# Performance work log

Hardware: AMD Instinct MI355X
Metric: run time of the kernel (lower is better)

Reference implementation:

```python
import jax, jax.numpy as jnp
import numpy as np

# Static conv hyperparameters (match init_kwargs)
STRIDE = (1, 1)
PAD = (1, 1)
DIL = (1, 1)
GROUPS = 1
DG = 1  # num_deformable_groups


def setup_inputs() -> dict:
    key = jax.random.key(0)
    k1, k2, k3 = jax.random.split(key, 3)
    B, C, H, W = 4, 256, 64, 64
    OC, kh, kw = 256, 3, 3
    x = jax.random.normal(k1, (B, C, H, W), dtype=jnp.float32)
    # offset: [B, DG*2*kh*kw, Ho, Wo], ordered (tap, [dy, dx]) per deformable group
    offset = jax.random.normal(k2, (B, DG * 2 * kh * kw, H, W), dtype=jnp.float32)
    n = C * kh * kw
    stdv = 1.0 / np.sqrt(n)
    weight = jax.random.uniform(k3, (OC, C // GROUPS, kh, kw), dtype=jnp.float32,
                                minval=-stdv, maxval=stdv)
    return {"x": x, "offset": offset, "weight": weight}


def _deform_conv(x, offset, weight):
    B, C, H, W = x.shape
    OC, Cg_w, kh, kw = weight.shape
    sh, sw = STRIDE
    ph, pw = PAD
    dh, dw = DIL
    Ho = (H + 2 * ph - (dh * (kh - 1) + 1)) // sh + 1
    Wo = (W + 2 * pw - (dw * (kw - 1) + 1)) // sw + 1
    K = kh * kw
    Cg = C // DG  # channels per deformable group

    # offsets: [B, DG, K, 2, Ho, Wo]; channel 0 = dy (h), channel 1 = dx (w)
    off = offset.reshape(B, DG, K, 2, Ho, Wo)

    # base (undeformed) sampling positions per tap
    ki, kj = jnp.meshgrid(jnp.arange(kh), jnp.arange(kw), indexing='ij')
    base_h = (jnp.arange(Ho) * sh - ph)[None, :] + (ki.reshape(-1) * dh)[:, None]  # [K, Ho]
    base_w = (jnp.arange(Wo) * sw - pw)[None, :] + (kj.reshape(-1) * dw)[:, None]  # [K, Wo]

    pos_h = base_h[None, None, :, :, None].astype(x.dtype) + off[:, :, :, 0]  # [B,DG,K,Ho,Wo]
    pos_w = base_w[None, None, :, None, :].astype(x.dtype) + off[:, :, :, 1]  # [B,DG,K,Ho,Wo]

    h0f = jnp.floor(pos_h)
    w0f = jnp.floor(pos_w)
    lh = pos_h - h0f  # fractional parts
    lw = pos_w - w0f
    h0 = h0f.astype(jnp.int32)
    w0 = w0f.astype(jnp.int32)

    xg = x.reshape(B, DG, Cg, H * W)

    def gather(hi, wi):
        # zero-padded gather: out-of-range corners contribute 0 (mmcv DCNv1 semantics)
        valid = (hi >= 0) & (hi < H) & (wi >= 0) & (wi < W)  # [B,DG,K,Ho,Wo]
        idx = jnp.clip(hi, 0, H - 1) * W + jnp.clip(wi, 0, W - 1)
        flat = idx.reshape(B, DG, 1, K * Ho * Wo)
        vals = jnp.take_along_axis(
            xg, jnp.broadcast_to(flat, (B, DG, Cg, K * Ho * Wo)), axis=3)
        vals = vals.reshape(B, DG, Cg, K, Ho, Wo)
        return vals * valid[:, :, None].astype(x.dtype)

    # bilinear interpolation over 4 corners -> im2col columns [B,DG,Cg,K,Ho,Wo]
    cols = (gather(h0, w0) * ((1 - lh) * (1 - lw))[:, :, None]
            + gather(h0, w0 + 1) * ((1 - lh) * lw)[:, :, None]
            + gather(h0 + 1, w0) * (lh * (1 - lw))[:, :, None]
            + gather(h0 + 1, w0 + 1) * (lh * lw)[:, :, None])

    # grouped GEMM: columns x weight
    cols = cols.reshape(B, GROUPS, C // GROUPS, K, Ho, Wo)
    wg = weight.reshape(GROUPS, OC // GROUPS, Cg_w, K)
    out = jnp.einsum('gock,bgckhw->bgohw', wg, cols)
    return out.reshape(B, OC, Ho, Wo)


def reference(x, offset, weight):
    return _deform_conv(x, offset, weight)
```

## Files before the change

kernel.cpp:

```cpp
#include <hip/hip_runtime.h>
#include <hip/hip_bf16.h>
#include <math.h>


constexpr int B  = 4;
constexpr int C  = 256;
constexpr int H  = 64;
constexpr int W  = 64;
constexpr int OC = 256;
constexpr int Ho = 64;
constexpr int Wo = 64;

constexpr int NT     = 64;
constexpr int CHUNKS = 72;
constexpr int WROW   = 40;

constexpr size_t WA_ELTS  = (size_t)CHUNKS * OC * WROW;
constexpr size_t XB_ELTS  = (size_t)B * 8 * 4096 * 32;
constexpr size_t OUT_ELTS = (size_t)B * OC * Ho * Wo;

typedef __attribute__((ext_vector_type(8))) short bf16x8;
typedef __attribute__((ext_vector_type(4))) float f32x4;

__device__ __forceinline__ float bf_lo(unsigned u) {
    union { unsigned i; float f; } c; c.i = u << 16; return c.f;
}
__device__ __forceinline__ float bf_hi(unsigned u) {
    union { unsigned i; float f; } c; c.i = u & 0xffff0000u; return c.f;
}
__device__ __forceinline__ ushort fbf(float f) {
    __hip_bfloat16 h = __float2bfloat16(f); return *(ushort*)&h;
}

__global__ __launch_bounds__(256)
void prep_all(const float* __restrict__ x, const float* __restrict__ wt,
              ushort* __restrict__ xb, ushort* __restrict__ wA)
{
    __shared__ ushort sx[128 * WROW];
    __shared__ ushort sw[CHUNKS * WROW];
    const int t = threadIdx.x;

    if (blockIdx.x < 1024) {
        const int blk = blockIdx.x;
        const int hwb = blk & 31;
        const int cb  = (blk >> 5) & 7;
        const int b   = blk >> 8;
        const int hw0 = hwb << 7;
        const int lhw = t & 127, chalf = t >> 7;
        #pragma unroll
        for (int i = 0; i < 16; ++i) {
            const int c = i * 2 + chalf;
            sx[lhw * WROW + c] =
                fbf(x[(((size_t)(b * 256 + cb * 32 + c)) << 12) + hw0 + lhw]);
        }
        __syncthreads();
        const int whw = t >> 1, wh = t & 1;
        const uint4 v0 = *(const uint4*)&sx[whw * WROW + wh * 16];
        const uint4 v1 = *(const uint4*)&sx[whw * WROW + wh * 16 + 8];
        uint4* dst = (uint4*)(xb + ((size_t)((b * 8 + cb) * 4096 + hw0) << 5));
        dst[whw * 4 + wh * 2 + 0] = v0;
        dst[whw * 4 + wh * 2 + 1] = v1;
    } else {
        const int oc = blockIdx.x - 1024;
        const int c  = t, chb = c >> 5, kk = c & 31;
        const float* wp = wt + ((size_t)oc * C + c) * 9;
        #pragma unroll
        for (int tap = 0; tap < 9; ++tap)
            sw[(tap * 8 + chb) * WROW + kk] = fbf(wp[tap]);
        if (c < CHUNKS) {
            #pragma unroll
            for (int j = 0; j < 8; ++j) sw[c * WROW + 32 + j] = 0;
        }
        __syncthreads();
        const uint4* sv = (const uint4*)sw;
        for (int i = c; i < CHUNKS * 5; i += 256) {
            const int row = i / 5, q = i % 5;
            ((uint4*)(wA + ((size_t)row * OC + oc) * WROW))[q] = sv[i];
        }
    }
}

__global__ __launch_bounds__(512, 1)
void dcn_mfma(const ushort* __restrict__ xb, const float* __restrict__ off,
              const ushort* __restrict__ wA_g, float* __restrict__ po)
{
    __shared__ __align__(16) ushort s_wA[OC * WROW];
    __shared__ __align__(16) ushort s_col[NT * WROW];
    __shared__ int2   s_midx[9 * NT];
    __shared__ float4 s_mw[9 * NT];

    const int xcd = blockIdx.x & 7;
    const int ii  = blockIdx.x >> 3;
    const int b   = xcd & 3;
    const int khalf = ii & 1;
    const int ho  = ((xcd >> 2) << 5) + (ii >> 1);
    const int ch0 = khalf * 36, ch1 = ch0 + 36;
    float* outp = po + (size_t)khalf * OUT_ELTS;
    const int tid = threadIdx.x;

    for (int s = tid; s < 9 * NT; s += 512) {
        const int n   = s & 63;
        const int tap = s >> 6;
        const float dy = off[((size_t)(b * 18 + 2 * tap)     * Ho + ho) * Wo + n];
        const float dx = off[((size_t)(b * 18 + 2 * tap + 1) * Ho + ho) * Wo + n];
        const float ph = (float)(ho - 1 + tap / 3) + dy;
        const float pw = (float)(n  - 1 + tap % 3) + dx;
        const float h0f = floorf(ph), w0f = floorf(pw);
        const int h0 = (int)h0f, w0 = (int)w0f;
        const float lh = ph - h0f, lw = pw - w0f;
        const int wb = min(max(w0, 0), W - 2);
        const int ht = min(max(h0, 0), H - 1);
        const int hb = min(max(h0 + 1, 0), H - 1);
        const float s0 = (wb == w0) ? (1.f - lw) : ((wb == w0 + 1) ? lw : 0.f);
        const float s1 = (wb + 1 == w0 + 1) ? lw : ((wb + 1 == w0) ? (1.f - lw) : 0.f);
        const float wtp = (h0 >= 0 && h0 < H)         ? (1.f - lh) : 0.f;
        const float wbt = (h0 + 1 >= 0 && h0 + 1 < H) ? lh         : 0.f;
        s_midx[s] = make_int2(ht * W + wb, hb * W + wb);
        s_mw[s]   = make_float4(wtp * s0, wtp * s1, wbt * s0, wbt * s1);
    }

    const int lane = tid & 63;
    const int wv   = tid >> 6;
    const int ocb  = wv >> 1;
    const int phh  = wv & 1;
    const int kq   = lane >> 4;
    const int mr   = lane & 15;

    const int sm_tid = tid - 256;
    const int sn  = sm_tid >> 2;
    const int sgg = sm_tid & 3;

    f32x4 acc[4][2];
    #pragma unroll
    for (int mt = 0; mt < 4; ++mt)
        #pragma unroll
        for (int nt = 0; nt < 2; ++nt)
            acc[mt][nt] = (f32x4){0.f, 0.f, 0.f, 0.f};

    for (int ch = ch0; ch < ch1; ++ch) {
        __syncthreads();

        if (tid < 256) {
            #pragma unroll
            for (int i = 0; i < 5; ++i) {
                const int seg = wv * 5 + i;
                __builtin_amdgcn_global_load_lds(
                    (const __attribute__((address_space(1))) void*)
                        (wA_g + (size_t)ch * OC * WROW + seg * 512 + lane * 8),
                    (__attribute__((address_space(3))) void*)&s_wA[seg * 512],
                    16, 0, 0);
            }
        } else {
            const int tap = ch >> 3;
            const int cb  = ch & 7;
            const int2   mi = s_midx[tap * NT + sn];
            const float4 mw = s_mw[tap * NT + sn];
            const ushort* xp = xb + ((size_t)(b * 8 + cb) << 17) + (sgg << 3);
            const uint4 c00 = *(const uint4*)(xp + ((size_t)mi.x << 5));
            const uint4 c01 = *(const uint4*)(xp + (((size_t)mi.x + 1) << 5));
            const uint4 c10 = *(const uint4*)(xp + ((size_t)mi.y << 5));
            const uint4 c11 = *(const uint4*)(xp + (((size_t)mi.y + 1) << 5));
            union { ushort pk[8]; uint4 v; } u;
            const unsigned a00[4] = {c00.x, c00.y, c00.z, c00.w};
            const unsigned a01[4] = {c01.x, c01.y, c01.z, c01.w};
            const unsigned a10[4] = {c10.x, c10.y, c10.z, c10.w};
            const unsigned a11[4] = {c11.x, c11.y, c11.z, c11.w};
            #pragma unroll
            for (int j = 0; j < 4; ++j) {
                const float vlo = mw.x * bf_lo(a00[j]) + mw.y * bf_lo(a01[j])
                                + mw.z * bf_lo(a10[j]) + mw.w * bf_lo(a11[j]);
                const float vhi = mw.x * bf_hi(a00[j]) + mw.y * bf_hi(a01[j])
                                + mw.z * bf_hi(a10[j]) + mw.w * bf_hi(a11[j]);
                u.pk[2 * j]     = fbf(vlo);
                u.pk[2 * j + 1] = fbf(vhi);
            }
            *(uint4*)&s_col[sn * WROW + sgg * 8] = u.v;
        }
        __syncthreads();

        bf16x8 bfr[2];
        #pragma unroll
        for (int nt = 0; nt < 2; ++nt)
            bfr[nt] = *(const bf16x8*)&s_col[((phh * 2 + nt) * 16 + mr) * WROW + kq * 8];
        #pragma unroll
        for (int mt = 0; mt < 4; ++mt) {
            const bf16x8 afr = *(const bf16x8*)&s_wA[(ocb * 64 + mt * 16 + mr) * WROW + kq * 8];
            #pragma unroll
            for (int nt = 0; nt < 2; ++nt)
                acc[mt][nt] = __builtin_amdgcn_mfma_f32_16x16x32_bf16(afr, bfr[nt], acc[mt][nt], 0, 0, 0);
        }
    }

    #pragma unroll
    for (int mt = 0; mt < 4; ++mt)
        #pragma unroll
        for (int nt = 0; nt < 2; ++nt)
            #pragma unroll
            for (int r = 0; r < 4; ++r) {
                const int oc = ocb * 64 + mt * 16 + kq * 4 + r;
                const int wo = (phh * 2 + nt) * 16 + mr;
                outp[((size_t)(b * OC + oc) * Ho + ho) * Wo + wo] = acc[mt][nt][r];
            }
}

__global__ __launch_bounds__(256)
void reduce2(const float4* __restrict__ p0, const float4* __restrict__ p1,
             float4* __restrict__ out)
{
    const int i = blockIdx.x * 256 + threadIdx.x;
    const float4 a = p0[i], b = p1[i];
    out[i] = make_float4(a.x + b.x, a.y + b.y, a.z + b.z, a.w + b.w);
}

extern "C" void kernel_launch(void* const* d_in, const int* in_sizes, int n_in,
                              void* d_out, int out_size, void* d_ws, size_t ws_size,
                              hipStream_t stream)
{
    const float* x   = (const float*)d_in[0];
    const float* off = (const float*)d_in[1];
    const float* wt  = (const float*)d_in[2];
    float* out = (float*)d_out;

    ushort* wA = (ushort*)d_ws;
    ushort* xb = wA + WA_ELTS;
    float*  po = (float*)(xb + XB_ELTS);

    prep_all<<<1280, 256, 0, stream>>>(x, wt, xb, wA);
    dcn_mfma<<<512, 512, 0, stream>>>(xb, off, wA, po);
    reduce2<<<(int)(OUT_ELTS / 4 / 256), 256, 0, stream>>>(
        (const float4*)po, (const float4*)(po + OUT_ELTS), (float4*)out);
}
```

Before: 120.9 us.

## Double-buffer weight DMA and gather staging with register prefetch pipeline

Splits the per-chunk loop into a two-stage software pipeline. Weights are DMA'd into alternating LDS buffers one chunk ahead, and sampler threads issue the next chunk's global gathers into registers before interpolating the current one. Fixed waitcnt counts, raw s_barrier and sched_barrier replace __syncthreads so loads overlap the MFMA phase. Launch bounds are raised to allow more blocks per CU despite doubled LDS use, which adds register pressure and relies on hand-tuned vmcnt values being correct.

Result: no change. 121.6 us (+0.6%).

```diff
diff --git a/kernel.cpp b/kernel.cpp
--- a/kernel.cpp
+++ b/kernel.cpp
@@ -80,21 +80,23 @@
     }
 }
 
-__global__ __launch_bounds__(512, 1)
+struct GathRegs { uint4 c00, c01, c10, c11; float4 mw; };
+
+__global__ __launch_bounds__(512, 4)
 void dcn_mfma(const ushort* __restrict__ xb, const float* __restrict__ off,
               const ushort* __restrict__ wA_g, float* __restrict__ po)
 {
-    __shared__ __align__(16) ushort s_wA[OC * WROW];
-    __shared__ __align__(16) ushort s_col[NT * WROW];
-    __shared__ int2   s_midx[9 * NT];
-    __shared__ float4 s_mw[9 * NT];
+    __shared__ __align__(16) ushort s_wA[2][OC * WROW];
+    __shared__ __align__(16) ushort s_col[2][NT * WROW];
+    __shared__ __align__(16) float4 s_mw[9 * NT];
+    __shared__ __align__(8)  int2   s_midx[9 * NT];
 
     const int xcd = blockIdx.x & 7;
     const int ii  = blockIdx.x >> 3;
     const int b   = xcd & 3;
     const int khalf = ii & 1;
     const int ho  = ((xcd >> 2) << 5) + (ii >> 1);
-    const int ch0 = khalf * 36, ch1 = ch0 + 36;
+    const int ch0 = khalf * 36;
     float* outp = po + (size_t)khalf * OUT_ELTS;
     const int tid = threadIdx.x;
 
@@ -125,10 +127,12 @@
     const int phh  = wv & 1;
     const int kq   = lane >> 4;
     const int mr   = lane & 15;
+    const bool is_w = (tid < 256);
 
     const int sm_tid = tid - 256;
     const int sn  = sm_tid >> 2;
     const int sgg = sm_tid & 3;
+    const ushort* xb_sg = xb + ((size_t)b << 20) + (sgg << 3);
 
     f32x4 acc[4][2];
     #pragma unroll
@@ -137,58 +141,97 @@
         for (int nt = 0; nt < 2; ++nt)
             acc[mt][nt] = (f32x4){0.f, 0.f, 0.f, 0.f};
 
-    for (int ch = ch0; ch < ch1; ++ch) {
-        __syncthreads();
-
-        if (tid < 256) {
-            #pragma unroll
-            for (int i = 0; i < 5; ++i) {
-                const int seg = wv * 5 + i;
-                __builtin_amdgcn_global_load_lds(
-                    (const __attribute__((address_space(1))) void*)
-                        (wA_g + (size_t)ch * OC * WROW + seg * 512 + lane * 8),
-                    (__attribute__((address_space(3))) void*)&s_wA[seg * 512],
-                    16, 0, 0);
+    auto dmaw = [&](int ch, int buf) {
+        #pragma unroll
+        for (int i = 0; i < 5; ++i) {
+            const int seg = wv * 5 + i;
+            __builtin_amdgcn_global_load_lds(
+                (const __attribute__((address_space(1))) void*)
+                    (wA_g + (size_t)ch * OC * WROW + seg * 512 + lane * 8),
+                (__attribute__((address_space(3))) void*)&s_wA[buf][seg * 512],
+                16, 0, 0);
+        }
+    };
+    auto issueg = [&](int ch, GathRegs& g) {
+        const int tap = ch >> 3;
+        const int cb  = ch & 7;
+        const int2 mi = s_midx[tap * NT + sn];
+        g.mw = s_mw[tap * NT + sn];
+        const ushort* xp = xb_sg + ((size_t)cb << 17);
+        g.c00 = *(const uint4*)(xp + ((size_t)mi.x << 5));
+        g.c01 = *(const uint4*)(xp + (((size_t)mi.x + 1) << 5));
+        g.c10 = *(const uint4*)(xp + ((size_t)mi.y << 5));
+        g.c11 = *(const uint4*)(xp + (((size_t)mi.y + 1) << 5));
+    };
+    auto sampfma = [&](const GathRegs& g, int buf) {
+        union { ushort pk[8]; uint4 v; } u;
+        const unsigned a00[4] = {g.c00.x, g.c00.y, g.c00.z, g.c00.w};
+        const unsigned a01[4] = {g.c01.x, g.c01.y, g.c01.z, g.c01.w};
+        const unsigned a10[4] = {g.c10.x, g.c10.y, g.c10.z, g.c10.w};
+        const unsigned a11[4] = {g.c11.x, g.c11.y, g.c11.z, g.c11.w};
+        #pragma unroll
+        for (int j = 0; j < 4; ++j) {
+            const float vlo = g.mw.x * bf_lo(a00[j]) + g.mw.y * bf_lo(a01[j])
+                            + g.mw.z * bf_lo(a10[j]) + g.mw.w * bf_lo(a11[j]);
+            const float vhi = g.mw.x * bf_hi(a00[j]) + g.mw.y * bf_hi(a01[j])
+                            + g.mw.z * bf_hi(a10[j]) + g.mw.w * bf_hi(a11[j]);
+            u.pk[2 * j]     = fbf(vlo);
+            u.pk[2 * j + 1] = fbf(vhi);
+        }
+        *(uint4*)&s_col[buf][sn * WROW + sgg * 8] = u.v;
+    };
+    auto mfmaph = [&](int buf) {
+        const bf16x8 bfr0 = *(const bf16x8*)&s_col[buf][((phh * 2 + 0) * 16 + mr) * WROW + kq * 8];
+        const bf16x8 bfr1 = *(const bf16x8*)&s_col[buf][((phh * 2 + 1) * 16 + mr) * WROW + kq * 8];
+        #pragma unroll
+        for (int mt = 0; mt < 4; ++mt) {
+            const bf16x8 afr = *(const bf16x8*)&s_wA[buf][(ocb * 64 + mt * 16 + mr) * WROW + kq * 8];
+            acc[mt][0] = __builtin_amdgcn_mfma_f32_16x16x32_bf16(afr, bfr0, acc[mt][0], 0, 0, 0);
+            acc[mt][1] = __builtin_amdgcn_mfma_f32_16x16x32_bf16(afr, bfr1, acc[mt][1], 0, 0, 0);
+        }
+    };
+
+    __syncthreads();
+
+    GathRegs gA, gB;
+    if (is_w) dmaw(ch0, 0);
+    else      issueg(ch0, gA);
+
+    #pragma unroll 1
+    for (int it = 0; it < 18; ++it) {
+        const int ch = ch0 + 2 * it;
+
+        if (is_w) {
+            dmaw(ch + 1, 1);
+            asm volatile("s_waitcnt vmcnt(5)" ::: "memory");
+        } else {
+            issueg(ch + 1, gB);
+            sampfma(gA, 0);
+            asm volatile("s_waitcnt lgkmcnt(0)" ::: "memory");
+        }
+        __builtin_amdgcn_s_barrier();
+        __builtin_amdgcn_sched_barrier(0);
+        mfmaph(0);
+        __builtin_amdgcn_sched_barrier(0);
+        __builtin_amdgcn_s_barrier();
+
+        if (is_w) {
+            if (it < 17) {
+                dmaw(ch + 2, 0);
+                asm volatile("s_waitcnt vmcnt(5)" ::: "memory");
+            } else {
+                asm volatile("s_waitcnt vmcnt(0)" ::: "memory");
             }
         } else {
-            const int tap = ch >> 3;
-            const int cb  = ch & 7;
-            const int2   mi = s_midx[tap * NT + sn];
-            const float4 mw = s_mw[tap * NT + sn];
-            const ushort* xp = xb + ((size_t)(b * 8 + cb) << 17) + (sgg << 3);
-            const uint4 c00 = *(const uint4*)(xp + ((size_t)mi.x << 5));
-            const uint4 c01 = *(const uint4*)(xp + (((size_t)mi.x + 1) << 5));
-            const uint4 c10 = *(const uint4*)(xp + ((size_t)mi.y << 5));
-            const uint4 c11 = *(const uint4*)(xp + (((size_t)mi.y + 1) << 5));
-            union { ushort pk[8]; uint4 v; } u;
-            const unsigned a00[4] = {c00.x, c00.y, c00.z, c00.w};
-            const unsigned a01[4] = {c01.x, c01.y, c01.z, c01.w};
-            const unsigned a10[4] = {c10.x, c10.y, c10.z, c10.w};
-            const unsigned a11[4] = {c11.x, c11.y, c11.z, c11.w};
-            #pragma unroll
-            for (int j = 0; j < 4; ++j) {
-                const float vlo = mw.x * bf_lo(a00[j]) + mw.y * bf_lo(a01[j])
-                                + mw.z * bf_lo(a10[j]) + mw.w * bf_lo(a11[j]);
-                const float vhi = mw.x * bf_hi(a00[j]) + mw.y * bf_hi(a01[j])
-                                + mw.z * bf_hi(a10[j]) + mw.w * bf_hi(a11[j]);
-                u.pk[2 * j]     = fbf(vlo);
-                u.pk[2 * j + 1] = fbf(vhi);
-            }
-            *(uint4*)&s_col[sn * WROW + sgg * 8] = u.v;
-        }
-        __syncthreads();
-
-        bf16x8 bfr[2];
-        #pragma unroll
-        for (int nt = 0; nt < 2; ++nt)
-            bfr[nt] = *(const bf16x8*)&s_col[((phh * 2 + nt) * 16 + mr) * WROW + kq * 8];
-        #pragma unroll
-        for (int mt = 0; mt < 4; ++mt) {
-            const bf16x8 afr = *(const bf16x8*)&s_wA[(ocb * 64 + mt * 16 + mr) * WROW + kq * 8];
-            #pragma unroll
-            for (int nt = 0; nt < 2; ++nt)
-                acc[mt][nt] = __builtin_amdgcn_mfma_f32_16x16x32_bf16(afr, bfr[nt], acc[mt][nt], 0, 0, 0);
-        }
+            if (it < 17) issueg(ch + 2, gA);
+            sampfma(gB, 1);
+            asm volatile("s_waitcnt lgkmcnt(0)" ::: "memory");
+        }
+        __builtin_amdgcn_s_barrier();
+        __builtin_amdgcn_sched_barrier(0);
+        mfmaph(1);
+        __builtin_amdgcn_sched_barrier(0);
+        __builtin_amdgcn_s_barrier();
     }
 
     #pragma unroll
```
